# Kernel optimization log

Measured on AMD Instinct MI355X. Metric: run time of the kernel, lower is better.

## Reference

```python
import jax, jax.numpy as jnp
import numpy as np

N_NODES = 50000
N_EDGES = 800000
IN_CH, HID_CH, OUT_CH = 128, 256, 16
GRAPH_SIZE = 50
NEG_SLOPE_ATT = 0.2   # GATConv attention leaky_relu slope
NEG_SLOPE_ACT = 0.01  # F.leaky_relu default between layers


def setup_inputs() -> dict:
    key = jax.random.key(0)
    ks = jax.random.split(key, 16)
    x = jax.random.normal(ks[0], (N_NODES, IN_CH), dtype=jnp.float32)
    edge_src = jax.random.randint(ks[1], (N_EDGES,), 0, N_NODES, dtype=jnp.int32)
    edge_dst = jax.random.randint(ks[2], (N_EDGES,), 0, N_NODES, dtype=jnp.int32)
    batch = (jnp.arange(N_NODES, dtype=jnp.int32) // GRAPH_SIZE).astype(jnp.int32)

    def mk(k, shape):
        return (jax.random.normal(k, shape, dtype=jnp.float32) * 0.1)

    # layer 1: 128 -> 256, layer 2: 256 -> 256, layer 3: 256 -> 16
    return {
        "x": x, "edge_src": edge_src, "edge_dst": edge_dst, "batch": batch,
        "W1": mk(ks[3], (IN_CH, HID_CH)), "a_src1": mk(ks[4], (HID_CH,)),
        "a_dst1": mk(ks[5], (HID_CH,)), "b1": jnp.zeros((HID_CH,), jnp.float32),
        "W2": mk(ks[6], (HID_CH, HID_CH)), "a_src2": mk(ks[7], (HID_CH,)),
        "a_dst2": mk(ks[8], (HID_CH,)), "b2": jnp.zeros((HID_CH,), jnp.float32),
        "W3": mk(ks[9], (HID_CH, OUT_CH)), "a_src3": mk(ks[10], (OUT_CH,)),
        "a_dst3": mk(ks[11], (OUT_CH,)), "b3": jnp.zeros((OUT_CH,), jnp.float32),
    }


def gat_conv(x, W, a_s, a_d, b, src, dst, n):
    # PyG GATConv (heads=1, add_self_loops=False, aggr='add')
    h = x @ W                                             # [N, F]
    s_src = h @ a_s                                       # [N]
    s_dst = h @ a_d                                       # [N]
    e = jax.nn.leaky_relu(s_src[src] + s_dst[dst], NEG_SLOPE_ATT)  # [E]
    m = jax.ops.segment_max(e, dst, num_segments=n)       # per-dst max
    ex = jnp.exp(e - m[dst])
    denom = jax.ops.segment_sum(ex, dst, num_segments=n)
    alpha = ex / denom[dst]                               # [E]
    out = jax.ops.segment_sum(alpha[:, None] * h[src], dst, num_segments=n)
    return out + b, alpha


def reference(x, edge_src, edge_dst, batch,
              W1, a_src1, a_dst1, b1,
              W2, a_src2, a_dst2, b2,
              W3, a_src3, a_dst3, b3):
    n = x.shape[0]
    h, _ = gat_conv(x, W1, a_src1, a_dst1, b1, edge_src, edge_dst, n)
    h = jax.nn.leaky_relu(h, NEG_SLOPE_ACT)  # dropout p=0.0 is a no-op
    h, _ = gat_conv(h, W2, a_src2, a_dst2, b2, edge_src, edge_dst, n)
    h = jax.nn.leaky_relu(h, NEG_SLOPE_ACT)
    h, alpha = gat_conv(h, W3, a_src3, a_dst3, b3, edge_src, edge_dst, n)
    # zero-node mask: first node of each graph (batch is sorted segment ids)
    zero_mask = jnp.concatenate([jnp.array([True]), batch[1:] != batch[:-1]])
    return h[zero_mask, :]
```

## Files before the change

kernel.cpp:

```cpp
#include <hip/hip_runtime.h>

#define NEG_ATT 0.2f
#define NEG_ACT 0.01f

typedef short s16x8 __attribute__((ext_vector_type(8)));
typedef float f32x4 __attribute__((ext_vector_type(4)));

__device__ __forceinline__ short f2bf_rn(float f) {
  unsigned u = __float_as_uint(f);
  unsigned r = (u + 0x7FFFu + ((u >> 16) & 1u)) >> 16;
  return (short)r;
}
__device__ __forceinline__ float bf2f(short h) {
  return __uint_as_float(((unsigned)(unsigned short)h) << 16);
}

__global__ __launch_bounds__(256) void conv_x(const float* __restrict__ X,
    short* __restrict__ Xb, int M, int K) {
  long long gid = (long long)blockIdx.x * 256 + threadIdx.x;
  long long tot = (long long)M * (K / 4);
  if (gid >= tot) return;
  int row = (int)(gid / (K / 4));
  int c4 = ((int)(gid % (K / 4))) * 4;
  float4 v = *(const float4*)&X[(size_t)row * K + c4];
  short4 hi, lo;
  hi.x = f2bf_rn(v.x); lo.x = f2bf_rn(v.x - bf2f(hi.x));
  hi.y = f2bf_rn(v.y); lo.y = f2bf_rn(v.y - bf2f(hi.y));
  hi.z = f2bf_rn(v.z); lo.z = f2bf_rn(v.z - bf2f(hi.z));
  hi.w = f2bf_rn(v.w); lo.w = f2bf_rn(v.w - bf2f(hi.w));
  *(short4*)&Xb[(size_t)row * 2 * K + c4] = hi;
  *(short4*)&Xb[(size_t)row * 2 * K + K + c4] = lo;
}

__global__ __launch_bounds__(256) void conv_w(const float* __restrict__ W,
    short* __restrict__ Wtb, int K, int N) {
  int gid = blockIdx.x * 256 + threadIdx.x;
  if (gid >= K * N) return;
  int k = gid / N, n = gid % N;
  float v = W[(size_t)k * N + n];
  short hi = f2bf_rn(v);
  short lo = f2bf_rn(v - bf2f(hi));
  Wtb[(size_t)n * 2 * K + k] = hi;
  Wtb[(size_t)n * 2 * K + K + k] = lo;
}

__global__ __launch_bounds__(256) void gemm_bf16split(const short* __restrict__ Xb,
    const short* __restrict__ Wtb, short* __restrict__ Cb, int M, int N, int K, int ldc) {
  __shared__ short sA[2][64][40];
  __shared__ short sB[2][64][40];
  const int K2 = 2 * K;
  int tid = threadIdx.x;
  int w = tid >> 6, l = tid & 63;
  int wr = w >> 1, wc = w & 1;
  int bm = blockIdx.y * 64, bn = blockIdx.x * 64;
  int sr = tid >> 2, sq = (tid & 3) * 8;

  f32x4 acc[2][2];
#pragma unroll
  for (int i = 0; i < 2; i++)
#pragma unroll
    for (int j = 0; j < 2; j++) acc[i][j] = (f32x4)0.f;

  int lrow = l & 15, k8 = (l >> 4) * 8;

  for (int k0 = 0; k0 < K; k0 += 32) {
    {
      int g = bm + sr;
      s16x8 hi = (s16x8)0, lo = (s16x8)0;
      if (g < M) {
        hi = *(const s16x8*)&Xb[(size_t)g * K2 + k0 + sq];
        lo = *(const s16x8*)&Xb[(size_t)g * K2 + K + k0 + sq];
      }
      *(s16x8*)&sA[0][sr][sq] = hi;
      *(s16x8*)&sA[1][sr][sq] = lo;
    }
    {
      int g = bn + sr;
      *(s16x8*)&sB[0][sr][sq] = *(const s16x8*)&Wtb[(size_t)g * K2 + k0 + sq];
      *(s16x8*)&sB[1][sr][sq] = *(const s16x8*)&Wtb[(size_t)g * K2 + K + k0 + sq];
    }
    __syncthreads();

    s16x8 aH[2], aL[2], bH[2], bL[2];
#pragma unroll
    for (int mt = 0; mt < 2; mt++) {
      aH[mt] = *(const s16x8*)&sA[0][wr * 32 + mt * 16 + lrow][k8];
      aL[mt] = *(const s16x8*)&sA[1][wr * 32 + mt * 16 + lrow][k8];
    }
#pragma unroll
    for (int nt = 0; nt < 2; nt++) {
      bH[nt] = *(const s16x8*)&sB[0][wc * 32 + nt * 16 + lrow][k8];
      bL[nt] = *(const s16x8*)&sB[1][wc * 32 + nt * 16 + lrow][k8];
    }
#pragma unroll
    for (int mt = 0; mt < 2; mt++)
#pragma unroll
      for (int nt = 0; nt < 2; nt++) {
        acc[mt][nt] = __builtin_amdgcn_mfma_f32_16x16x32_bf16(aH[mt], bH[nt], acc[mt][nt], 0, 0, 0);
        acc[mt][nt] = __builtin_amdgcn_mfma_f32_16x16x32_bf16(aH[mt], bL[nt], acc[mt][nt], 0, 0, 0);
        acc[mt][nt] = __builtin_amdgcn_mfma_f32_16x16x32_bf16(aL[mt], bH[nt], acc[mt][nt], 0, 0, 0);
      }
    __syncthreads();
  }

  int dcol = l & 15, drow4 = (l >> 4) * 4;
#pragma unroll
  for (int mt = 0; mt < 2; mt++)
#pragma unroll
    for (int nt = 0; nt < 2; nt++) {
      int col = bn + wc * 32 + nt * 16 + dcol;
      if (col < N) {
#pragma unroll
        for (int r = 0; r < 4; r++) {
          int row = bm + wr * 32 + mt * 16 + drow4 + r;
          if (row < M) Cb[(size_t)row * ldc + col] = f2bf_rn(acc[mt][nt][r]);
        }
      }
    }
}

__global__ __launch_bounds__(256) void row_dots(const short* __restrict__ Hb,
    const float* __restrict__ a_s, const float* __restrict__ a_d,
    float* __restrict__ s_src, float* __restrict__ s_dst, int Nn, int F, int ld) {
  int node = blockIdx.x * 4 + (threadIdx.x >> 6);
  int lane = threadIdx.x & 63;
  if (node >= Nn) return;
  float ss = 0.f, sd = 0.f;
  for (int c = lane; c < F; c += 64) {
    float h = bf2f(Hb[(size_t)node * ld + c]);
    ss += h * a_s[c];
    sd += h * a_d[c];
  }
#pragma unroll
  for (int off = 32; off > 0; off >>= 1) {
    ss += __shfl_down(ss, off);
    sd += __shfl_down(sd, off);
  }
  if (lane == 0) { s_src[node] = ss; s_dst[node] = sd; }
}

__global__ __launch_bounds__(256) void deg_hist(const int* __restrict__ dst,
    int* __restrict__ deg, int E) {
  int e = blockIdx.x * 256 + threadIdx.x;
  if (e >= E) return;
  atomicAdd(&deg[dst[e]], 1);
}

__global__ __launch_bounds__(256) void scan_partials(const int* __restrict__ deg,
    int* __restrict__ bsum, int N) {
  __shared__ int sdata[256];
  int i = blockIdx.x * 256 + threadIdx.x;
  sdata[threadIdx.x] = (i < N) ? deg[i] : 0;
  __syncthreads();
  for (int off = 128; off > 0; off >>= 1) {
    if (threadIdx.x < off) sdata[threadIdx.x] += sdata[threadIdx.x + off];
    __syncthreads();
  }
  if (threadIdx.x == 0) bsum[blockIdx.x] = sdata[0];
}

__global__ __launch_bounds__(256) void scan_offsets(int* __restrict__ bsum, int nb) {
  __shared__ int sdata[256];
  __shared__ int carry;
  int tid = threadIdx.x;
  if (tid == 0) carry = 0;
  __syncthreads();
  for (int base = 0; base < nb; base += 256) {
    int idx = base + tid;
    int v = (idx < nb) ? bsum[idx] : 0;
    sdata[tid] = v;
    __syncthreads();
    for (int off = 1; off < 256; off <<= 1) {
      int t = (tid >= off) ? sdata[tid - off] : 0;
      __syncthreads();
      sdata[tid] += t;
      __syncthreads();
    }
    if (idx < nb) bsum[idx] = carry + sdata[tid] - v;
    __syncthreads();
    if (tid == 255) carry += sdata[255];
    __syncthreads();
  }
}

__global__ __launch_bounds__(256) void scan_final(const int* __restrict__ deg,
    const int* __restrict__ bsum, int* __restrict__ rowptr, int N, int E) {
  __shared__ int sdata[256];
  int i = blockIdx.x * 256 + threadIdx.x;
  int tid = threadIdx.x;
  int v = (i < N) ? deg[i] : 0;
  sdata[tid] = v;
  __syncthreads();
  for (int off = 1; off < 256; off <<= 1) {
    int t = (tid >= off) ? sdata[tid - off] : 0;
    __syncthreads();
    sdata[tid] += t;
    __syncthreads();
  }
  if (i < N) rowptr[i] = bsum[blockIdx.x] + sdata[tid] - v;
  if (blockIdx.x == 0 && tid == 0) rowptr[N] = E;
}

__global__ __launch_bounds__(256) void csr_place(const int* __restrict__ src,
    const int* __restrict__ dst, const int* __restrict__ rowptr,
    int* __restrict__ cnt, int* __restrict__ csr_src, int E) {
  int e = blockIdx.x * 256 + threadIdx.x;
  if (e >= E) return;
  int d = dst[e];
  int pos = rowptr[d] + atomicAdd(&cnt[d], 1);
  csr_src[pos] = src[e];
}

__global__ __launch_bounds__(256) void attn_agg256(const short* __restrict__ Hb,
    const float* __restrict__ ssrc, const float* __restrict__ sdst,
    const int* __restrict__ rowptr, const int* __restrict__ csr_src,
    const float* __restrict__ b, short* __restrict__ outb, int N, float slope) {
  int node = blockIdx.x * 4 + (threadIdx.x >> 6);
  int lane = threadIdx.x & 63;
  if (node >= N) return;
  int r0 = rowptr[node], r1 = rowptr[node + 1];
  float sd = sdst[node];
  int c4 = lane * 4;
  float x0 = 0.f, y0 = 0.f, z0 = 0.f, w0 = 0.f;
  float x1 = 0.f, y1 = 0.f, z1 = 0.f, w1 = 0.f;
  float s = 0.f;
  int i = r0;
  for (; i + 2 <= r1; i += 2) {
    int s0 = csr_src[i], s1 = csr_src[i + 1];
    float v0 = ssrc[s0] + sd; v0 = v0 > 0.f ? v0 : v0 * NEG_ATT;
    float v1 = ssrc[s1] + sd; v1 = v1 > 0.f ? v1 : v1 * NEG_ATT;
    float a0 = expf(v0), a1 = expf(v1);
    s += a0 + a1;
    short4 h0 = *(const short4*)&Hb[(size_t)s0 * 256 + c4];
    short4 h1 = *(const short4*)&Hb[(size_t)s1 * 256 + c4];
    x0 += a0 * bf2f(h0.x); y0 += a0 * bf2f(h0.y);
    z0 += a0 * bf2f(h0.z); w0 += a0 * bf2f(h0.w);
    x1 += a1 * bf2f(h1.x); y1 += a1 * bf2f(h1.y);
    z1 += a1 * bf2f(h1.z); w1 += a1 * bf2f(h1.w);
  }
  if (i < r1) {
    int s0 = csr_src[i];
    float v0 = ssrc[s0] + sd; v0 = v0 > 0.f ? v0 : v0 * NEG_ATT;
    float a0 = expf(v0);
    s += a0;
    short4 h0 = *(const short4*)&Hb[(size_t)s0 * 256 + c4];
    x0 += a0 * bf2f(h0.x); y0 += a0 * bf2f(h0.y);
    z0 += a0 * bf2f(h0.z); w0 += a0 * bf2f(h0.w);
  }
  float inv = 1.f / s;
  float4 bias = *(const float4*)&b[c4];
  float vx = (x0 + x1) * inv + bias.x, vy = (y0 + y1) * inv + bias.y;
  float vz = (z0 + z1) * inv + bias.z, vw = (w0 + w1) * inv + bias.w;
  if (r0 == r1) { vx = bias.x; vy = bias.y; vz = bias.z; vw = bias.w; }
  vx = vx > 0.f ? vx : vx * slope;
  vy = vy > 0.f ? vy : vy * slope;
  vz = vz > 0.f ? vz : vz * slope;
  vw = vw > 0.f ? vw : vw * slope;
  short4 hi, lo;
  hi.x = f2bf_rn(vx); lo.x = f2bf_rn(vx - bf2f(hi.x));
  hi.y = f2bf_rn(vy); lo.y = f2bf_rn(vy - bf2f(hi.y));
  hi.z = f2bf_rn(vz); lo.z = f2bf_rn(vz - bf2f(hi.z));
  hi.w = f2bf_rn(vw); lo.w = f2bf_rn(vw - bf2f(hi.w));
  *(short4*)&outb[(size_t)node * 512 + c4] = hi;
  *(short4*)&outb[(size_t)node * 512 + 256 + c4] = lo;
}

__global__ __launch_bounds__(256) void attn_agg16(const short* __restrict__ Hb,
    const float* __restrict__ ssrc, const float* __restrict__ sdst,
    const int* __restrict__ rowptr, const int* __restrict__ csr_src,
    const float* __restrict__ b, const int* __restrict__ batch,
    float* __restrict__ out, int N, int ld) {
  int node = blockIdx.x * 4 + (threadIdx.x >> 6);
  int lane = threadIdx.x & 63;
  if (node >= N) return;
  if (node != 0 && batch[node] == batch[node - 1]) return;
  int r0 = rowptr[node], r1 = rowptr[node + 1];
  float sd = sdst[node];
  int c = lane & 15, eg = lane >> 4;
  float acc = 0.f, s = 0.f;
  for (int i = r0 + eg; i < r1; i += 4) {
    int sn = csr_src[i];
    float v = ssrc[sn] + sd;
    v = v > 0.f ? v : v * NEG_ATT;
    float a = expf(v);
    s += a;
    acc += a * bf2f(Hb[(size_t)sn * ld + c]);
  }
#pragma unroll
  for (int off = 16; off < 64; off <<= 1) {
    acc += __shfl_xor(acc, off);
    s += __shfl_xor(s, off);
  }
  if (eg == 0) {
    float v = (r0 == r1) ? b[c] : acc / s + b[c];
    out[(size_t)batch[node] * 16 + c] = v;
  }
}

extern "C" void kernel_launch(void* const* d_in, const int* in_sizes, int n_in,
                              void* d_out, int out_size, void* d_ws, size_t ws_size,
                              hipStream_t stream) {
  const float* x   = (const float*)d_in[0];
  const int* src   = (const int*)d_in[1];
  const int* dst   = (const int*)d_in[2];
  const int* batch = (const int*)d_in[3];
  const float* W1 = (const float*)d_in[4];
  const float* as1 = (const float*)d_in[5];
  const float* ad1 = (const float*)d_in[6];
  const float* b1 = (const float*)d_in[7];
  const float* W2 = (const float*)d_in[8];
  const float* as2 = (const float*)d_in[9];
  const float* ad2 = (const float*)d_in[10];
  const float* b2 = (const float*)d_in[11];
  const float* W3 = (const float*)d_in[12];
  const float* as3 = (const float*)d_in[13];
  const float* ad3 = (const float*)d_in[14];
  const float* b3 = (const float*)d_in[15];

  const int N = in_sizes[3];
  const int E = in_sizes[1];

  char* ws = (char*)d_ws;
  size_t off = 0;
  auto alloc = [&](size_t bytes) -> void* {
    void* p = ws + off;
    off = (off + bytes + 255) & ~(size_t)255;
    return p;
  };
  short* Hb     = (short*)alloc((size_t)N * 256 * 2);
  short* Xb     = (short*)alloc((size_t)N * 512 * 2);
  float* ssrc   = (float*)alloc((size_t)N * 4);
  float* sdst   = (float*)alloc((size_t)N * 4);
  int* deg      = (int*)alloc((size_t)N * 4);
  int* rowptr   = (int*)alloc((size_t)(N + 1) * 4);
  int* cnt      = (int*)alloc((size_t)N * 4);
  int* csr_src  = (int*)alloc((size_t)E * 4);
  int* bsum     = (int*)alloc((size_t)1024 * 4);
  short* W1tb   = (short*)alloc((size_t)256 * 256 * 2);
  short* W2tb   = (short*)alloc((size_t)256 * 512 * 2);
  short* W3tb   = (short*)alloc((size_t)64 * 512 * 2);
  (void)ws_size;

  dim3 blk(256);
  int eblocks = (E + 255) / 256;
  int nblocks = (N + 255) / 256;
  int gblocksY = (N + 63) / 64;
  int nb4 = (N + 3) / 4;

  conv_w<<<(128 * 256 + 255) / 256, blk, 0, stream>>>(W1, W1tb, 128, 256);
  conv_w<<<(256 * 256 + 255) / 256, blk, 0, stream>>>(W2, W2tb, 256, 256);
  (void)hipMemsetAsync(W3tb, 0, (size_t)64 * 512 * 2, stream);
  conv_w<<<(256 * 16 + 255) / 256, blk, 0, stream>>>(W3, W3tb, 256, 16);
  conv_x<<<(int)(((long long)N * 32 + 255) / 256), blk, 0, stream>>>(x, Xb, N, 128);
  (void)hipMemsetAsync(deg, 0, (size_t)N * 4, stream);
  deg_hist<<<eblocks, blk, 0, stream>>>(dst, deg, E);
  scan_partials<<<nblocks, blk, 0, stream>>>(deg, bsum, N);
  scan_offsets<<<1, blk, 0, stream>>>(bsum, nblocks);
  scan_final<<<nblocks, blk, 0, stream>>>(deg, bsum, rowptr, N, E);
  (void)hipMemsetAsync(cnt, 0, (size_t)N * 4, stream);
  csr_place<<<eblocks, blk, 0, stream>>>(src, dst, rowptr, cnt, csr_src, E);

  gemm_bf16split<<<dim3(4, gblocksY), blk, 0, stream>>>(Xb, W1tb, Hb, N, 256, 128, 256);
  row_dots<<<nb4, blk, 0, stream>>>(Hb, as1, ad1, ssrc, sdst, N, 256, 256);
  attn_agg256<<<nb4, blk, 0, stream>>>(Hb, ssrc, sdst, rowptr, csr_src, b1, Xb, N, NEG_ACT);

  gemm_bf16split<<<dim3(4, gblocksY), blk, 0, stream>>>(Xb, W2tb, Hb, N, 256, 256, 256);
  row_dots<<<nb4, blk, 0, stream>>>(Hb, as2, ad2, ssrc, sdst, N, 256, 256);
  attn_agg256<<<nb4, blk, 0, stream>>>(Hb, ssrc, sdst, rowptr, csr_src, b2, Xb, N, NEG_ACT);

  gemm_bf16split<<<dim3(1, gblocksY), blk, 0, stream>>>(Xb, W3tb, Hb, N, 64, 256, 64);
  row_dots<<<nb4, blk, 0, stream>>>(Hb, as3, ad3, ssrc, sdst, N, 16, 64);
  attn_agg16<<<nb4, blk, 0, stream>>>(Hb, ssrc, sdst, rowptr, csr_src, b3, batch,
                                      (float*)d_out, N, 64);
}
```

Measured before the change: 375.3 us.

## Fuse attention score dots into larger 128x128 GEMM tile epilogue

Grows the bf16-split MFMA GEMM tile from 64x64 with 256 threads to 128x128 with 512 threads. For layers 1 and 2 it computes the per-node source and destination attention dot products inside the GEMM epilogue, using a wave shuffle reduction and atomicAdd into zeroed buffers, so the separate row_dots pass over H goes away. Layer 3 drops the zero padding of N from 64 to 16 and adds a bounds check instead. The trade-offs are atomics, extra memsets, and wasted tile work when N=16 inside a 128-wide tile.

```diff
diff --git a/kernel.cpp b/kernel.cpp
--- a/kernel.cpp
+++ b/kernel.cpp
@@ -44,20 +44,23 @@
   Wtb[(size_t)n * 2 * K + K + k] = lo;
 }
 
-__global__ __launch_bounds__(256) void gemm_bf16split(const short* __restrict__ Xb,
-    const short* __restrict__ Wtb, short* __restrict__ Cb, int M, int N, int K, int ldc) {
-  __shared__ short sA[2][64][40];
-  __shared__ short sB[2][64][40];
+__global__ __launch_bounds__(512) void gemm128(const short* __restrict__ Xb,
+    const short* __restrict__ Wtb, short* __restrict__ Cb,
+    const float* __restrict__ a_s, const float* __restrict__ a_d,
+    float* __restrict__ ssrc, float* __restrict__ sdst,
+    int M, int N, int K, int ldc) {
+  __shared__ short sA[2][128][40];
+  __shared__ short sB[2][128][40];
   const int K2 = 2 * K;
   int tid = threadIdx.x;
   int w = tid >> 6, l = tid & 63;
-  int wr = w >> 1, wc = w & 1;
-  int bm = blockIdx.y * 64, bn = blockIdx.x * 64;
+  int wr = w >> 2, wc = w & 3;
+  int bm = blockIdx.y * 128, bn = blockIdx.x * 128;
   int sr = tid >> 2, sq = (tid & 3) * 8;
 
-  f32x4 acc[2][2];
-#pragma unroll
-  for (int i = 0; i < 2; i++)
+  f32x4 acc[4][2];
+#pragma unroll
+  for (int i = 0; i < 4; i++)
 #pragma unroll
     for (int j = 0; j < 2; j++) acc[i][j] = (f32x4)0.f;
 
@@ -76,16 +79,21 @@
     }
     {
       int g = bn + sr;
-      *(s16x8*)&sB[0][sr][sq] = *(const s16x8*)&Wtb[(size_t)g * K2 + k0 + sq];
-      *(s16x8*)&sB[1][sr][sq] = *(const s16x8*)&Wtb[(size_t)g * K2 + K + k0 + sq];
-    }
-    __syncthreads();
-
-    s16x8 aH[2], aL[2], bH[2], bL[2];
-#pragma unroll
-    for (int mt = 0; mt < 2; mt++) {
-      aH[mt] = *(const s16x8*)&sA[0][wr * 32 + mt * 16 + lrow][k8];
-      aL[mt] = *(const s16x8*)&sA[1][wr * 32 + mt * 16 + lrow][k8];
+      s16x8 hi = (s16x8)0, lo = (s16x8)0;
+      if (g < N) {
+        hi = *(const s16x8*)&Wtb[(size_t)g * K2 + k0 + sq];
+        lo = *(const s16x8*)&Wtb[(size_t)g * K2 + K + k0 + sq];
+      }
+      *(s16x8*)&sB[0][sr][sq] = hi;
+      *(s16x8*)&sB[1][sr][sq] = lo;
+    }
+    __syncthreads();
+
+    s16x8 aH[4], aL[4], bH[2], bL[2];
+#pragma unroll
+    for (int mt = 0; mt < 4; mt++) {
+      aH[mt] = *(const s16x8*)&sA[0][wr * 64 + mt * 16 + lrow][k8];
+      aL[mt] = *(const s16x8*)&sA[1][wr * 64 + mt * 16 + lrow][k8];
     }
 #pragma unroll
     for (int nt = 0; nt < 2; nt++) {
@@ -93,7 +101,7 @@
       bL[nt] = *(const s16x8*)&sB[1][wc * 32 + nt * 16 + lrow][k8];
     }
 #pragma unroll
-    for (int mt = 0; mt < 2; mt++)
+    for (int mt = 0; mt < 4; mt++)
 #pragma unroll
       for (int nt = 0; nt < 2; nt++) {
         acc[mt][nt] = __builtin_amdgcn_mfma_f32_16x16x32_bf16(aH[mt], bH[nt], acc[mt][nt], 0, 0, 0);
@@ -105,18 +113,46 @@
 
   int dcol = l & 15, drow4 = (l >> 4) * 4;
 #pragma unroll
-  for (int mt = 0; mt < 2; mt++)
+  for (int mt = 0; mt < 4; mt++) {
+    float ps[4] = {0.f, 0.f, 0.f, 0.f}, pd[4] = {0.f, 0.f, 0.f, 0.f};
 #pragma unroll
     for (int nt = 0; nt < 2; nt++) {
       int col = bn + wc * 32 + nt * 16 + dcol;
       if (col < N) {
+        float asc = 0.f, adc = 0.f;
+        if (a_s) { asc = a_s[col]; adc = a_d[col]; }
 #pragma unroll
         for (int r = 0; r < 4; r++) {
-          int row = bm + wr * 32 + mt * 16 + drow4 + r;
-          if (row < M) Cb[(size_t)row * ldc + col] = f2bf_rn(acc[mt][nt][r]);
+          int row = bm + wr * 64 + mt * 16 + drow4 + r;
+          if (row < M) {
+            float v = acc[mt][nt][r];
+            Cb[(size_t)row * ldc + col] = f2bf_rn(v);
+            ps[r] += v * asc; pd[r] += v * adc;
+          }
         }
       }
     }
+    if (a_s) {
+#pragma unroll
+      for (int m = 1; m < 16; m <<= 1) {
+#pragma unroll
+        for (int r = 0; r < 4; r++) {
+          ps[r] += __shfl_xor(ps[r], m);
+          pd[r] += __shfl_xor(pd[r], m);
+        }
+      }
+      if ((l & 15) == 0) {
+#pragma unroll
+        for (int r = 0; r < 4; r++) {
+          int row = bm + wr * 64 + mt * 16 + drow4 + r;
+          if (row < M) {
+            atomicAdd(&ssrc[row], ps[r]);
+            atomicAdd(&sdst[row], pd[r]);
+          }
+        }
+      }
+    }
+  }
 }
 
 __global__ __launch_bounds__(256) void row_dots(const short* __restrict__ Hb,
@@ -338,18 +374,17 @@
   int* bsum     = (int*)alloc((size_t)1024 * 4);
   short* W1tb   = (short*)alloc((size_t)256 * 256 * 2);
   short* W2tb   = (short*)alloc((size_t)256 * 512 * 2);
-  short* W3tb   = (short*)alloc((size_t)64 * 512 * 2);
+  short* W3tb   = (short*)alloc((size_t)16 * 512 * 2);
   (void)ws_size;
 
   dim3 blk(256);
   int eblocks = (E + 255) / 256;
   int nblocks = (N + 255) / 256;
-  int gblocksY = (N + 63) / 64;
+  int g128 = (N + 127) / 128;
   int nb4 = (N + 3) / 4;
 
   conv_w<<<(128 * 256 + 255) / 256, blk, 0, stream>>>(W1, W1tb, 128, 256);
   conv_w<<<(256 * 256 + 255) / 256, blk, 0, stream>>>(W2, W2tb, 256, 256);
-  (void)hipMemsetAsync(W3tb, 0, (size_t)64 * 512 * 2, stream);
   conv_w<<<(256 * 16 + 255) / 256, blk, 0, stream>>>(W3, W3tb, 256, 16);
   conv_x<<<(int)(((long long)N * 32 + 255) / 256), blk, 0, stream>>>(x, Xb, N, 128);
   (void)hipMemsetAsync(deg, 0, (size_t)N * 4, stream);
@@ -360,16 +395,21 @@
   (void)hipMemsetAsync(cnt, 0, (size_t)N * 4, stream);
   csr_place<<<eblocks, blk, 0, stream>>>(src, dst, rowptr, cnt, csr_src, E);
 
-  gemm_bf16split<<<dim3(4, gblocksY), blk, 0, stream>>>(Xb, W1tb, Hb, N, 256, 128, 256);
-  row_dots<<<nb4, blk, 0, stream>>>(Hb, as1, ad1, ssrc, sdst, N, 256, 256);
+  (void)hipMemsetAsync(ssrc, 0, (size_t)N * 4, stream);
+  (void)hipMemsetAsync(sdst, 0, (size_t)N * 4, stream);
+  gemm128<<<dim3(2, g128), dim3(512), 0, stream>>>(Xb, W1tb, Hb, as1, ad1, ssrc, sdst,
+                                                   N, 256, 128, 256);
   attn_agg256<<<nb4, blk, 0, stream>>>(Hb, ssrc, sdst, rowptr, csr_src, b1, Xb, N, NEG_ACT);
 
-  gemm_bf16split<<<dim3(4, gblocksY), blk, 0, stream>>>(Xb, W2tb, Hb, N, 256, 256, 256);
-  row_dots<<<nb4, blk, 0, stream>>>(Hb, as2, ad2, ssrc, sdst, N, 256, 256);
+  (void)hipMemsetAsync(ssrc, 0, (size_t)N * 4, stream);
+  (void)hipMemsetAsync(sdst, 0, (size_t)N * 4, stream);
+  gemm128<<<dim3(2, g128), dim3(512), 0, stream>>>(Xb, W2tb, Hb, as2, ad2, ssrc, sdst,
+                                                   N, 256, 256, 256);
   attn_agg256<<<nb4, blk, 0, stream>>>(Hb, ssrc, sdst, rowptr, csr_src, b2, Xb, N, NEG_ACT);
 
-  gemm_bf16split<<<dim3(1, gblocksY), blk, 0, stream>>>(Xb, W3tb, Hb, N, 64, 256, 64);
-  row_dots<<<nb4, blk, 0, stream>>>(Hb, as3, ad3, ssrc, sdst, N, 16, 64);
+  gemm128<<<dim3(1, g128), dim3(512), 0, stream>>>(Xb, W3tb, Hb, nullptr, nullptr,
+                                                   nullptr, nullptr, N, 16, 256, 16);
+  row_dots<<<nb4, blk, 0, stream>>>(Hb, as3, ad3, ssrc, sdst, N, 16, 16);
   attn_agg16<<<nb4, blk, 0, stream>>>(Hb, ssrc, sdst, rowptr, csr_src, b3, batch,
-                                      (float*)d_out, N, 64);
-}
+                                      (float*)d_out, N, 16);
+}
```

After: 384.2 us. 2.4% more time.
